# Kernel optimization log

Hardware: AMD Instinct MI355X
Metric: run time of the kernel (lower is better)

The kernel has to match this reference:

```python
import jax, jax.numpy as jnp
import numpy as np

NP_, NA_, NS_ = 4096, 4096, 1
E_ = 131072
DIN, DOUT, H = 256, 64, 4
SLOPE = 0.2  # leaky relu negative slope


def _leaky(x):
    return jnp.where(x >= 0, x, SLOPE * x)


def setup_inputs() -> dict:
    key = jax.random.key(0)
    ks = iter(jax.random.split(key, 64))
    inp = {}
    inp['feat_P'] = jax.random.normal(next(ks), (NP_, DIN), jnp.float32)
    inp['feat_A'] = jax.random.normal(next(ks), (NA_, DIN), jnp.float32)
    inp['feat_state'] = jax.random.normal(next(ks), (NS_, DIN), jnp.float32)
    for name in ['P', 'A', 'p2p', 'p2a', 'a2p', 'a2a', 'p2s', 'a2s', 'in']:
        inp['W_' + name] = jax.random.normal(next(ks), (DOUT * H, DIN), jnp.float32) / np.sqrt(DIN)
        inp['b_' + name] = jax.random.normal(next(ks), (DOUT * H,), jnp.float32) * 0.01
    for name in ['p2p', 'p2a', 'a2p', 'a2a', 'p2s', 'a2s']:
        inp['att_%s_src' % name] = jax.random.normal(next(ks), (1, H, DOUT), jnp.float32) * 0.1
        inp['att_%s_dst' % name] = jax.random.normal(next(ks), (1, H, DOUT), jnp.float32) * 0.1
    for name, ns, nd in [('p2p', NP_, NP_), ('p2a', NP_, NA_), ('a2p', NA_, NP_), ('a2a', NA_, NA_)]:
        inp['e_%s_src' % name] = jax.random.randint(next(ks), (E_,), 0, ns, jnp.int32)
        inp['e_%s_dst' % name] = jax.random.randint(next(ks), (E_,), 0, nd, jnp.int32)
    inp['e_p2s_src'] = jnp.arange(NP_, dtype=jnp.int32)
    inp['e_p2s_dst'] = jnp.zeros((NP_,), jnp.int32)
    inp['e_a2s_src'] = jnp.arange(NA_, dtype=jnp.int32)
    inp['e_a2s_dst'] = jnp.zeros((NA_,), jnp.int32)
    return inp


def _msg_agg(feat_src, W, b, att_s, att_d, Wh_dst, src, dst, n_dst):
    # per-edge lossy_u_mul_e with comm_loss == 0 (noise branch dead):
    # gather src features, per-edge linear, per-edge softmax over HEADS (torch Softmax(dim=1)).
    h = feat_src[src]                                    # [E, DIN]
    Wh = (h @ W.T + b).reshape(-1, H, DOUT)              # [E, H, D]
    a_s = jnp.sum(Wh * att_s, axis=-1, keepdims=True)    # [E, H, 1]
    a_d = jnp.sum(Wh_dst[dst] * att_d, axis=-1, keepdims=True)
    attn = jax.nn.softmax(_leaky(a_s + a_d), axis=1)     # softmax over heads, as in original
    return jax.ops.segment_sum(Wh * attn, dst, num_segments=n_dst)


def _edge_softmax_agg(Wh_src, att_s, Wh_state, att_d, src, dst, n_dst):
    # dgl edge_softmax: destination-grouped stable softmax over incoming edges.
    a_s = jnp.sum(Wh_src * att_s, axis=-1, keepdims=True)[src]    # [E, H, 1]
    a_d = jnp.sum(Wh_state * att_d, axis=-1, keepdims=True)[dst]  # [E, H, 1]
    e = _leaky(a_s + a_d)
    m = jax.ops.segment_max(e, dst, num_segments=n_dst)
    ex = jnp.exp(e - m[dst])
    den = jax.ops.segment_sum(ex, dst, num_segments=n_dst)
    a = ex / den[dst]
    return jax.ops.segment_sum(Wh_src[src] * a, dst, num_segments=n_dst)


def reference(feat_P, feat_A, feat_state,
              W_P, b_P, W_A, b_A, W_p2p, b_p2p, W_p2a, b_p2a, W_a2p, b_a2p,
              W_a2a, b_a2a, W_p2s, b_p2s, W_a2s, b_a2s, W_in, b_in,
              att_p2p_src, att_p2p_dst, att_p2a_src, att_p2a_dst,
              att_a2p_src, att_a2p_dst, att_a2a_src, att_a2a_dst,
              att_p2s_src, att_p2s_dst, att_a2s_src, att_a2s_dst,
              e_p2p_src, e_p2p_dst, e_p2a_src, e_p2a_dst,
              e_a2p_src, e_a2p_dst, e_a2a_src, e_a2a_dst,
              e_p2s_src, e_p2s_dst, e_a2s_src, e_a2s_dst):
    Whp = (feat_P @ W_P.T + b_P).reshape(NP_, H, DOUT)
    Wha = (feat_A @ W_A.T + b_A).reshape(NA_, H, DOUT)
    Whp2s = (feat_P @ W_p2s.T + b_p2s).reshape(NP_, H, DOUT)
    Wha2s = (feat_A @ W_a2s.T + b_a2s).reshape(NA_, H, DOUT)
    Whin = (feat_state @ W_in.T + b_in).reshape(NS_, H, DOUT)

    ft_p2p = _msg_agg(feat_P, W_p2p, b_p2p, att_p2p_src, att_p2p_dst, Whp, e_p2p_src, e_p2p_dst, NP_)
    ft_p2a = _msg_agg(feat_P, W_p2a, b_p2a, att_p2a_src, att_p2a_dst, Wha, e_p2a_src, e_p2a_dst, NA_)
    ft_a2p = _msg_agg(feat_A, W_a2p, b_a2p, att_a2p_src, att_a2p_dst, Whp, e_a2p_src, e_a2p_dst, NP_)
    ft_a2a = _msg_agg(feat_A, W_a2a, b_a2a, att_a2a_src, att_a2a_dst, Wha, e_a2a_src, e_a2a_dst, NA_)

    ft_p2s = _edge_softmax_agg(Whp2s, att_p2s_src, Whin, att_p2s_dst, e_p2s_src, e_p2s_dst, NS_)
    ft_a2s = _edge_softmax_agg(Wha2s, att_a2s_src, Whin, att_a2s_dst, e_a2s_src, e_a2s_dst, NS_)

    h_P = jax.nn.relu(Whp + ft_p2p + ft_a2p)
    h_A = jax.nn.relu(Wha + ft_p2a + ft_a2a)
    h_S = jax.nn.relu(Whin + ft_p2s + ft_a2s)
    return (h_P, h_A, h_S)
```

## Files before the change

### kernel.cpp

```cpp
#include <hip/hip_runtime.h>

#define NPA   4096
#define DHD   256
#define EDG   131072
#define OS    4104
#define TBL_SZ ((size_t)NPA * DHD)

#define B_AH    ((size_t)0)
#define B_WH    (B_AH + 2 * TBL_SZ * 2)
#define B_TBL   (B_WH + (size_t)8 * 65536 * 2)
#define B_SCORE (B_TBL + 8 * TBL_SZ * 2)
#define B_CNT   (B_SCORE + (size_t)10 * NPA * 4 * 4)
#define B_SCD   (B_CNT + (size_t)4 * NPA * 4)
#define B_DEN   (B_SCD + 8 * 4)
#define B_NUM   (B_DEN + 8 * 4)
#define B_ZEND  (B_NUM + 512 * 4)
#define B_OFFS  (B_ZEND)
#define B_CUR   (B_OFFS + (size_t)4 * OS * 4)
#define B_PKT   (B_CUR + (size_t)4 * NPA * 4)
#define B_WHIN  (B_PKT + (size_t)4 * EDG * 16)

typedef _Float16 half8 __attribute__((ext_vector_type(8)));
typedef _Float16 half4 __attribute__((ext_vector_type(4)));
typedef _Float16 half2v __attribute__((ext_vector_type(2)));
typedef float floatx4 __attribute__((ext_vector_type(4)));

struct CastArgs { const float* src[10]; };
struct GemmArgs {
    const float* b[8];
    const float* att0[8]; const float* att1[8];
    int sj0[8]; int sj1[8];
};
struct EdgeArgs { const int* src[4]; const int* dst[4]; };

__device__ __forceinline__ float lrelu(float x) { return x >= 0.0f ? x : 0.2f * x; }

__device__ __forceinline__ int pack2(float a, float b) {
    half2v h = {(_Float16)a, (_Float16)b};
    return __builtin_bit_cast(int, h);
}
__device__ __forceinline__ half2v bc2(int v) { return __builtin_bit_cast(half2v, v); }

__device__ __forceinline__ half2v asplat(const int4& p, int head) {
    int w = (head & 2) ? p.z : p.y;
    int b = (head & 1) ? ((w >> 16) & 0xffff) : (w & 0xffff);
    return bc2(b | (b << 16));
}

__global__ __launch_bounds__(256) void prep_kernel(CastArgs ca, EdgeArgs ea,
        const float* __restrict__ fs, const float* __restrict__ Win,
        const float* __restrict__ bin, const float* __restrict__ attP,
        const float* __restrict__ attA, _Float16* __restrict__ dst,
        int* __restrict__ cnt, float* __restrict__ whin, float* __restrict__ scd) {
    __shared__ int hist[NPA];
    int bid = blockIdx.x;
    int tid = threadIdx.x;
    if (bid < 32) {
        int r = bid >> 3;
        int chunk = bid & 7;
        const int* dp = ea.dst[r] + chunk * 16384;
#pragma unroll
        for (int i = 0; i < 16; ++i) hist[tid + i * 256] = 0;
        __syncthreads();
#pragma unroll
        for (int k = 0; k < 64; ++k)
            atomicAdd(&hist[dp[k * 256 + tid]], 1);
        __syncthreads();
        int* cr = cnt + r * NPA;
#pragma unroll
        for (int i = 0; i < 16; ++i) {
            int v = hist[tid + i * 256];
            if (v) atomicAdd(&cr[tid + i * 256], v);
        }
        return;
    }
    int wave = tid >> 6, lane = tid & 63;
    if (bid < 96) {
        int o = (bid - 32) * 4 + wave;
        float4 w = *(const float4*)&Win[(size_t)o * 256 + lane * 4];
        float4 f = *(const float4*)&fs[lane * 4];
        float v = w.x * f.x + w.y * f.y + w.z * f.z + w.w * f.w;
        for (int d = 32; d; d >>= 1) v += __shfl_xor(v, d);
        if (lane == 0) {
            v += bin[o];
            whin[o] = v;
            atomicAdd(&scd[o >> 6], v * attP[o]);
            atomicAdd(&scd[4 + (o >> 6)], v * attA[o]);
        }
        return;
    }
    size_t i4 = ((size_t)(bid - 96) * 256 + tid) * 4;
    const float* s; size_t off;
    if (i4 < TBL_SZ)            { s = ca.src[0]; off = i4; }
    else if (i4 < 2 * TBL_SZ)   { s = ca.src[1]; off = i4 - TBL_SZ; }
    else { size_t r = i4 - 2 * TBL_SZ; s = ca.src[2 + (r >> 16)]; off = r & 65535; }
    float4 v = *(const float4*)(s + off);
    half4 hh = {(_Float16)v.x, (_Float16)v.y, (_Float16)v.z, (_Float16)v.w};
    *(half4*)(dst + i4) = hh;
}

__global__ __launch_bounds__(256) void gemm_kernel(const _Float16* __restrict__ Ah,
        const _Float16* __restrict__ Whb, GemmArgs ga,
        _Float16* __restrict__ tblBase, float* __restrict__ score) {
    int j = blockIdx.x >> 6;
    int mt = blockIdx.x & 63;
    int w = threadIdx.x >> 6, lane = threadIdx.x & 63;
    int quad = lane >> 4, l16 = lane & 15;
    const _Float16* A = Ah + (size_t)(j >> 2) * TBL_SZ;
    const _Float16* W = Whb + (size_t)j * 65536;
    const float* bias = ga.b[j];
    _Float16* out = tblBase + (size_t)j * TBL_SZ;
    int mr0 = mt * 64;
    int nc0 = w * 64;
    const _Float16* ap[4];
    const _Float16* bp[4];
#pragma unroll
    for (int g = 0; g < 4; ++g) {
        ap[g] = A + (size_t)(mr0 + g * 16 + l16) * 256 + quad * 8;
        bp[g] = W + (size_t)(nc0 + g * 16 + l16) * 256 + quad * 8;
    }
    floatx4 acc[4][4];
#pragma unroll
    for (int rg = 0; rg < 4; ++rg)
#pragma unroll
        for (int cg = 0; cg < 4; ++cg) acc[rg][cg] = (floatx4){0, 0, 0, 0};
#pragma unroll
    for (int k0 = 0; k0 < 256; k0 += 32) {
        half8 av[4], bv[4];
#pragma unroll
        for (int g = 0; g < 4; ++g) av[g] = *(const half8*)(ap[g] + k0);
#pragma unroll
        for (int g = 0; g < 4; ++g) bv[g] = *(const half8*)(bp[g] + k0);
#pragma unroll
        for (int rg = 0; rg < 4; ++rg)
#pragma unroll
            for (int cg = 0; cg < 4; ++cg)
                acc[rg][cg] = __builtin_amdgcn_mfma_f32_16x16x32_f16(av[rg], bv[cg], acc[rg][cg], 0, 0, 0);
    }
    float bc[4];
#pragma unroll
    for (int cg = 0; cg < 4; ++cg) bc[cg] = bias[nc0 + cg * 16 + l16];
#pragma unroll
    for (int rg = 0; rg < 4; ++rg)
#pragma unroll
        for (int i = 0; i < 4; ++i) {
            int row = mr0 + rg * 16 + quad * 4 + i;
#pragma unroll
            for (int cg = 0; cg < 4; ++cg)
                out[(size_t)row * 256 + nc0 + cg * 16 + l16] = (_Float16)(acc[rg][cg][i] + bc[cg]);
        }
#pragma unroll
    for (int tt = 0; tt < 2; ++tt) {
        const float* att = tt ? ga.att1[j] : ga.att0[j];
        int sj = tt ? ga.sj1[j] : ga.sj0[j];
        if (!att) continue;
        float at[4];
#pragma unroll
        for (int cg = 0; cg < 4; ++cg) at[cg] = att[nc0 + cg * 16 + l16];
        float* sb = score + (size_t)sj * NPA * 4;
#pragma unroll
        for (int rg = 0; rg < 4; ++rg)
#pragma unroll
            for (int i = 0; i < 4; ++i) {
                float p = (acc[rg][0][i] + bc[0]) * at[0] + (acc[rg][1][i] + bc[1]) * at[1]
                        + (acc[rg][2][i] + bc[2]) * at[2] + (acc[rg][3][i] + bc[3]) * at[3];
                p += __shfl_xor(p, 1); p += __shfl_xor(p, 2);
                p += __shfl_xor(p, 4); p += __shfl_xor(p, 8);
                if (l16 == 0) {
                    int row = mr0 + rg * 16 + quad * 4 + i;
                    sb[(size_t)row * 4 + w] = p;
                }
            }
    }
}

__global__ __launch_bounds__(1024) void scan_kernel(const int* __restrict__ counts,
                                                    int* __restrict__ offs, int* __restrict__ cur) {
    int r = blockIdx.x;
    int t = threadIdx.x;
    int wave = t >> 6, lane = t & 63;
    int4 v = *(const int4*)&counts[(size_t)r * NPA + t * 4];
    int lsum = v.x + v.y + v.z + v.w;
    int s = lsum;
#pragma unroll
    for (int d = 1; d < 64; d <<= 1) {
        int u = __shfl_up(s, d);
        if (lane >= d) s += u;
    }
    __shared__ int wsum[16];
    if (lane == 63) wsum[wave] = s;
    __syncthreads();
    if (wave == 0 && lane < 16) {
        int wv = wsum[lane];
#pragma unroll
        for (int d = 1; d < 16; d <<= 1) {
            int u = __shfl_up(wv, d);
            if (lane >= d) wv += u;
        }
        wsum[lane] = wv;
    }
    __syncthreads();
    int base = (wave ? wsum[wave - 1] : 0) + s - lsum;
    int4 ov = {base, base + v.x, base + v.x + v.y, base + v.x + v.y + v.z};
    *(int4*)&offs[(size_t)r * OS + t * 4] = ov;
    *(int4*)&cur[(size_t)r * NPA + t * 4] = ov;
    if (t == 1023) offs[(size_t)r * OS + NPA] = base + lsum;
}

__global__ __launch_bounds__(256) void scatter_attn(EdgeArgs ea, const float* __restrict__ scoreBase,
        int* __restrict__ cur, int4* __restrict__ pkt) {
    int idx = (blockIdx.x * 256 + threadIdx.x) * 2;
    int r = idx >> 17;
    int e = idx & (EDG - 1);
    int2 s2 = *(const int2*)&ea.src[r][e];
    int2 d2 = *(const int2*)&ea.dst[r][e];
    const float* as = scoreBase + (size_t)r * NPA * 4;
    const float* ad = scoreBase + (size_t)(4 + r) * NPA * 4;
    float4 av0 = *(const float4*)&as[(size_t)s2.x * 4];
    float4 dv0 = *(const float4*)&ad[(size_t)d2.x * 4];
    float4 av1 = *(const float4*)&as[(size_t)s2.y * 4];
    float4 dv1 = *(const float4*)&ad[(size_t)d2.y * 4];
#pragma unroll
    for (int u = 0; u < 2; ++u) {
        float4 av = u ? av1 : av0;
        float4 dv = u ? dv1 : dv0;
        int s = u ? s2.y : s2.x;
        int d = u ? d2.y : d2.x;
        float x0 = lrelu(av.x + dv.x), x1 = lrelu(av.y + dv.y);
        float x2 = lrelu(av.z + dv.z), x3 = lrelu(av.w + dv.w);
        float m = fmaxf(fmaxf(x0, x1), fmaxf(x2, x3));
        float e0 = __expf(x0 - m), e1 = __expf(x1 - m), e2 = __expf(x2 - m), e3 = __expf(x3 - m);
        float inv = 1.0f / (e0 + e1 + e2 + e3);
        int pos = atomicAdd(&cur[r * NPA + d], 1);
        int4 pk = {s, pack2(e0 * inv, e1 * inv), pack2(e2 * inv, e3 * inv), 0};
        pkt[(size_t)r * EDG + pos] = pk;
    }
}

__global__ __launch_bounds__(256) void agg_kernel(const int* __restrict__ offs,
        const int4* __restrict__ pkt, const _Float16* __restrict__ tblBase,
        float* __restrict__ outBase) {
    int side = blockIdx.y;
    int wave = threadIdx.x >> 6, lane = threadIdx.x & 63;
    int dn = blockIdx.x * 4 + wave;
    int h = lane >> 5, l32 = lane & 31;
    int head = l32 >> 3;
    half2v accA[4] = {{0,0},{0,0},{0,0},{0,0}};
    half2v accB[4] = {{0,0},{0,0},{0,0},{0,0}};
    const int srcIdx[4] = {1, 2, 5, 6};
    const int4 z = {0, 0, 0, 0};
#pragma unroll
    for (int q = 0; q < 2; ++q) {
        int r = side + q * 2;
        const int* of = offs + (size_t)r * OS;
        const int4* pkb = pkt + (size_t)r * EDG;
        const _Float16* wh = tblBase + (size_t)srcIdx[r] * TBL_SZ;
        int beg = of[dn], end = of[dn + 1];
        int i = beg;
        int4 p0 = (i + h     < end) ? pkb[i + h]     : z;
        int4 p1 = (i + 2 + h < end) ? pkb[i + 2 + h] : z;
        int4 p2 = (i + 4 + h < end) ? pkb[i + 4 + h] : z;
        int4 p3 = (i + 6 + h < end) ? pkb[i + 6 + h] : z;
        while (i < end) {
            int ni = i + 8;
            half8 w0 = *(const half8*)(wh + (size_t)p0.x * 256 + l32 * 8);
            half8 w1 = *(const half8*)(wh + (size_t)p1.x * 256 + l32 * 8);
            half8 w2 = *(const half8*)(wh + (size_t)p2.x * 256 + l32 * 8);
            half8 w3 = *(const half8*)(wh + (size_t)p3.x * 256 + l32 * 8);
            int4 n0 = (ni + h     < end) ? pkb[ni + h]     : z;
            int4 n1 = (ni + 2 + h < end) ? pkb[ni + 2 + h] : z;
            int4 n2 = (ni + 4 + h < end) ? pkb[ni + 4 + h] : z;
            int4 n3 = (ni + 6 + h < end) ? pkb[ni + 6 + h] : z;
            half2v a0 = asplat(p0, head), a1 = asplat(p1, head);
            half2v a2 = asplat(p2, head), a3 = asplat(p3, head);
            int4 i0 = __builtin_bit_cast(int4, w0);
            int4 i1 = __builtin_bit_cast(int4, w1);
            int4 i2 = __builtin_bit_cast(int4, w2);
            int4 i3 = __builtin_bit_cast(int4, w3);
            accA[0] += bc2(i0.x) * a0; accA[1] += bc2(i0.y) * a0;
            accA[2] += bc2(i0.z) * a0; accA[3] += bc2(i0.w) * a0;
            accB[0] += bc2(i1.x) * a1; accB[1] += bc2(i1.y) * a1;
            accB[2] += bc2(i1.z) * a1; accB[3] += bc2(i1.w) * a1;
            accA[0] += bc2(i2.x) * a2; accA[1] += bc2(i2.y) * a2;
            accA[2] += bc2(i2.z) * a2; accA[3] += bc2(i2.w) * a2;
            accB[0] += bc2(i3.x) * a3; accB[1] += bc2(i3.y) * a3;
            accB[2] += bc2(i3.z) * a3; accB[3] += bc2(i3.w) * a3;
            p0 = n0; p1 = n1; p2 = n2; p3 = n3;
            i = ni;
        }
    }
    float f[8];
#pragma unroll
    for (int k = 0; k < 4; ++k) {
        half2v s = accA[k] + accB[k];
        f[2 * k] = (float)s[0];
        f[2 * k + 1] = (float)s[1];
    }
#pragma unroll
    for (int k = 0; k < 8; ++k) f[k] += __shfl_xor(f[k], 32);
    if (h == 0) {
        const _Float16* skip = tblBase + (size_t)(side * 4) * TBL_SZ + (size_t)dn * 256 + l32 * 8;
        half8 sv = *(const half8*)skip;
        float* op = outBase + ((size_t)side * NPA + dn) * 256 + l32 * 8;
        float4 o0 = {fmaxf(f[0] + (float)sv[0], 0.f), fmaxf(f[1] + (float)sv[1], 0.f),
                     fmaxf(f[2] + (float)sv[2], 0.f), fmaxf(f[3] + (float)sv[3], 0.f)};
        float4 o1 = {fmaxf(f[4] + (float)sv[4], 0.f), fmaxf(f[5] + (float)sv[5], 0.f),
                     fmaxf(f[6] + (float)sv[6], 0.f), fmaxf(f[7] + (float)sv[7], 0.f)};
        *(float4*)op = o0;
        *(float4*)(op + 4) = o1;
    }
}

__global__ __launch_bounds__(256) void state_kernel(const _Float16* __restrict__ tblBase,
        const float* __restrict__ scoreBase, const float* __restrict__ scd,
        float* __restrict__ den, float* __restrict__ num) {
    int r = blockIdx.y;
    int blk = blockIdx.x;
    int t = threadIdx.x;
    int h = t >> 6;
    const _Float16* wh = tblBase + (size_t)(r == 0 ? 3 : 7) * TBL_SZ;
    const float* as = scoreBase + (size_t)(8 + r) * NPA * 4;
    float dh = scd[r * 4 + h];
    float dsum = 0.0f, acc = 0.0f;
    for (int i = blk; i < NPA; i += 128) {
        float x = lrelu(as[(size_t)i * 4 + h] + dh);
        float w = __expf(x);
        dsum += w;
        acc += w * (float)wh[(size_t)i * 256 + t];
    }
    atomicAdd(&num[r * 256 + t], acc);
    if ((t & 63) == 0) atomicAdd(&den[r * 4 + h], dsum);
}

__global__ __launch_bounds__(256) void state_final(const float* __restrict__ whin,
        const float* __restrict__ den, const float* __restrict__ num, float* __restrict__ out) {
    int t = threadIdx.x;
    int h = t >> 6;
    float v = whin[t] + num[t] / den[h] + num[256 + t] / den[4 + h];
    out[t] = v > 0.0f ? v : 0.0f;
}

extern "C" void kernel_launch(void* const* d_in, const int* in_sizes, int n_in,
                              void* d_out, int out_size, void* d_ws, size_t ws_size,
                              hipStream_t stream) {
    auto F = [&](int i) { return (const float*)d_in[i]; };
    char* ws = (char*)d_ws;
    _Float16* Ah  = (_Float16*)(ws + B_AH);
    _Float16* Whb = (_Float16*)(ws + B_WH);
    _Float16* tbl = (_Float16*)(ws + B_TBL);
    float* score  = (float*)(ws + B_SCORE);
    int* cnt      = (int*)(ws + B_CNT);
    float* scd    = (float*)(ws + B_SCD);
    float* den    = (float*)(ws + B_DEN);
    float* num    = (float*)(ws + B_NUM);
    int* offs     = (int*)(ws + B_OFFS);
    int* cur      = (int*)(ws + B_CUR);
    int4* pkt     = (int4*)(ws + B_PKT);
    float* whin   = (float*)(ws + B_WHIN);

    (void)hipMemsetAsync(ws + B_CNT, 0, B_ZEND - B_CNT, stream);

    CastArgs ca = {{F(0), F(1), F(3), F(7), F(9), F(15), F(5), F(11), F(13), F(17)}};
    EdgeArgs ea = {{(const int*)d_in[33], (const int*)d_in[35], (const int*)d_in[37], (const int*)d_in[39]},
                   {(const int*)d_in[34], (const int*)d_in[36], (const int*)d_in[38], (const int*)d_in[40]}};

    prep_kernel<<<2656, 256, 0, stream>>>(ca, ea, F(2), F(19), F(20), F(30), F(32),
                                          Ah, cnt, whin, scd);

    GemmArgs ga;
    const int bIdx[8] = {4, 8, 10, 16, 6, 12, 14, 18};
    for (int j = 0; j < 8; ++j) ga.b[j] = F(bIdx[j]);
    const int a0Idx[8]  = {22, 21, 23, 29, 24, 25, 27, 31};
    const int sj0Arr[8] = { 4,  0,  1,  8,  5,  2,  3,  9};
    for (int j = 0; j < 8; ++j) {
        ga.att0[j] = F(a0Idx[j]); ga.sj0[j] = sj0Arr[j];
        ga.att1[j] = nullptr;     ga.sj1[j] = -1;
    }
    ga.att1[0] = F(26); ga.sj1[0] = 6;
    ga.att1[4] = F(28); ga.sj1[4] = 7;

    gemm_kernel<<<512, 256, 0, stream>>>(Ah, Whb, ga, tbl, score);
    scan_kernel<<<4, 1024, 0, stream>>>(cnt, offs, cur);
    scatter_attn<<<1024, 256, 0, stream>>>(ea, score, cur, pkt);
    agg_kernel<<<dim3(1024, 2), 256, 0, stream>>>(offs, pkt, tbl, (float*)d_out);
    state_kernel<<<dim3(128, 2), 256, 0, stream>>>(tbl, score, scd, den, num);
    state_final<<<1, 256, 0, stream>>>(whin, den, num, (float*)d_out + 2 * TBL_SZ);
}
```

Measured before the change: 269.6 us.

## Fuse scan into GEMM, state into scatter/agg, drop memset and global atomics

Cuts the launch count from seven (memset plus six kernels) to four by merging kernels. The edge-count scan now runs inside the GEMM launch, the state reduction inside the scatter launch, and the state finalize inside the aggregation launch. Per-block histograms and partial state sums are written to private slots instead of being combined with global atomics, which removes the memset. The GEMM M-tile is halved to 32 rows, giving 1024 blocks for more parallelism. The trade-offs are extra partial-sum reads in the finalize step and the state-vector dot product shrinking to a single block.

```diff
diff --git a/kernel.cpp b/kernel.cpp
--- a/kernel.cpp
+++ b/kernel.cpp
@@ -4,21 +4,21 @@
 #define DHD   256
 #define EDG   131072
 #define OS    4104
+#define PST   64
 #define TBL_SZ ((size_t)NPA * DHD)
 
 #define B_AH    ((size_t)0)
 #define B_WH    (B_AH + 2 * TBL_SZ * 2)
 #define B_TBL   (B_WH + (size_t)8 * 65536 * 2)
 #define B_SCORE (B_TBL + 8 * TBL_SZ * 2)
-#define B_CNT   (B_SCORE + (size_t)10 * NPA * 4 * 4)
-#define B_SCD   (B_CNT + (size_t)4 * NPA * 4)
-#define B_DEN   (B_SCD + 8 * 4)
-#define B_NUM   (B_DEN + 8 * 4)
-#define B_ZEND  (B_NUM + 512 * 4)
-#define B_OFFS  (B_ZEND)
+#define B_CNTP  (B_SCORE + (size_t)10 * NPA * 4 * 4)
+#define B_OFFS  (B_CNTP + (size_t)32 * NPA * 4)
 #define B_CUR   (B_OFFS + (size_t)4 * OS * 4)
 #define B_PKT   (B_CUR + (size_t)4 * NPA * 4)
 #define B_WHIN  (B_PKT + (size_t)4 * EDG * 16)
+#define B_SCD   (B_WHIN + 256 * 4)
+#define B_NUMP  (B_SCD + 8 * 4)
+#define B_DENP  (B_NUMP + (size_t)2 * PST * 256 * 4)
 
 typedef _Float16 half8 __attribute__((ext_vector_type(8)));
 typedef _Float16 half4 __attribute__((ext_vector_type(4)));
@@ -51,7 +51,7 @@
         const float* __restrict__ fs, const float* __restrict__ Win,
         const float* __restrict__ bin, const float* __restrict__ attP,
         const float* __restrict__ attA, _Float16* __restrict__ dst,
-        int* __restrict__ cnt, float* __restrict__ whin, float* __restrict__ scd) {
+        int* __restrict__ cntp, float* __restrict__ whin, float* __restrict__ scd) {
     __shared__ int hist[NPA];
     int bid = blockIdx.x;
     int tid = threadIdx.x;
@@ -66,30 +66,30 @@
         for (int k = 0; k < 64; ++k)
             atomicAdd(&hist[dp[k * 256 + tid]], 1);
         __syncthreads();
-        int* cr = cnt + r * NPA;
-#pragma unroll
-        for (int i = 0; i < 16; ++i) {
-            int v = hist[tid + i * 256];
-            if (v) atomicAdd(&cr[tid + i * 256], v);
-        }
+        int* cr = cntp + (size_t)bid * NPA;
+#pragma unroll
+        for (int i = 0; i < 16; ++i)
+            cr[tid + i * 256] = hist[tid + i * 256];
         return;
     }
     int wave = tid >> 6, lane = tid & 63;
-    if (bid < 96) {
-        int o = (bid - 32) * 4 + wave;
-        float4 w = *(const float4*)&Win[(size_t)o * 256 + lane * 4];
-        float4 f = *(const float4*)&fs[lane * 4];
-        float v = w.x * f.x + w.y * f.y + w.z * f.z + w.w * f.w;
-        for (int d = 32; d; d >>= 1) v += __shfl_xor(v, d);
-        if (lane == 0) {
+    if (bid == 32) {
+        float sp = 0.f, sa = 0.f;
+        for (int k = 0; k < 64; ++k) {
+            int o = wave * 64 + k;
+            float4 w = *(const float4*)&Win[(size_t)o * 256 + lane * 4];
+            float4 f = *(const float4*)&fs[lane * 4];
+            float v = w.x * f.x + w.y * f.y + w.z * f.z + w.w * f.w;
+            for (int d = 32; d; d >>= 1) v += __shfl_xor(v, d);
             v += bin[o];
-            whin[o] = v;
-            atomicAdd(&scd[o >> 6], v * attP[o]);
-            atomicAdd(&scd[4 + (o >> 6)], v * attA[o]);
-        }
+            if (lane == 0) whin[o] = v;
+            sp += v * attP[o];
+            sa += v * attA[o];
+        }
+        if (lane == 0) { scd[wave] = sp; scd[4 + wave] = sa; }
         return;
     }
-    size_t i4 = ((size_t)(bid - 96) * 256 + tid) * 4;
+    size_t i4 = ((size_t)(bid - 33) * 256 + tid) * 4;
     const float* s; size_t off;
     if (i4 < TBL_SZ)            { s = ca.src[0]; off = i4; }
     else if (i4 < 2 * TBL_SZ)   { s = ca.src[1]; off = i4 - TBL_SZ; }
@@ -99,40 +99,90 @@
     *(half4*)(dst + i4) = hh;
 }
 
-__global__ __launch_bounds__(256) void gemm_kernel(const _Float16* __restrict__ Ah,
-        const _Float16* __restrict__ Whb, GemmArgs ga,
-        _Float16* __restrict__ tblBase, float* __restrict__ score) {
-    int j = blockIdx.x >> 6;
-    int mt = blockIdx.x & 63;
-    int w = threadIdx.x >> 6, lane = threadIdx.x & 63;
+__global__ __launch_bounds__(256) void gemm_scan(const _Float16* __restrict__ Ah,
+        const _Float16* __restrict__ Whb, GemmArgs ga, const int* __restrict__ cntp,
+        _Float16* __restrict__ tblBase, float* __restrict__ score,
+        int* __restrict__ offs, int* __restrict__ cur) {
+    int bid = blockIdx.x;
+    int t = threadIdx.x;
+    if (bid < 4) {
+        int r = bid;
+        int4 s[4];
+#pragma unroll
+        for (int q = 0; q < 4; ++q) {
+            int4 acc = {0, 0, 0, 0};
+#pragma unroll
+            for (int b = 0; b < 8; ++b) {
+                const int4* cp = (const int4*)(cntp + (size_t)(r * 8 + b) * NPA);
+                int4 u = cp[t * 4 + q];
+                acc.x += u.x; acc.y += u.y; acc.z += u.z; acc.w += u.w;
+            }
+            s[q] = acc;
+        }
+        int lsum = 0;
+#pragma unroll
+        for (int q = 0; q < 4; ++q) lsum += s[q].x + s[q].y + s[q].z + s[q].w;
+        int wave = t >> 6, lane = t & 63;
+        int sc = lsum;
+#pragma unroll
+        for (int d = 1; d < 64; d <<= 1) {
+            int u = __shfl_up(sc, d);
+            if (lane >= d) sc += u;
+        }
+        __shared__ int ws4[4];
+        if (lane == 63) ws4[wave] = sc;
+        __syncthreads();
+        int wb = 0;
+        for (int w = 0; w < 4; ++w) if (w < wave) wb += ws4[w];
+        int run = wb + sc - lsum;
+        int* of = offs + (size_t)r * OS;
+        int* cu = cur + (size_t)r * NPA;
+#pragma unroll
+        for (int q = 0; q < 4; ++q) {
+            int4 o;
+            o.x = run; run += s[q].x;
+            o.y = run; run += s[q].y;
+            o.z = run; run += s[q].z;
+            o.w = run; run += s[q].w;
+            ((int4*)of)[t * 4 + q] = o;
+            ((int4*)cu)[t * 4 + q] = o;
+        }
+        if (t == 255) of[NPA] = run;
+        return;
+    }
+    int g = bid - 4;
+    int j = g >> 7;
+    int mt = g & 127;
+    int w = t >> 6, lane = t & 63;
     int quad = lane >> 4, l16 = lane & 15;
     const _Float16* A = Ah + (size_t)(j >> 2) * TBL_SZ;
     const _Float16* W = Whb + (size_t)j * 65536;
     const float* bias = ga.b[j];
     _Float16* out = tblBase + (size_t)j * TBL_SZ;
-    int mr0 = mt * 64;
+    int mr0 = mt * 32;
     int nc0 = w * 64;
-    const _Float16* ap[4];
+    const _Float16* ap[2];
     const _Float16* bp[4];
 #pragma unroll
-    for (int g = 0; g < 4; ++g) {
-        ap[g] = A + (size_t)(mr0 + g * 16 + l16) * 256 + quad * 8;
-        bp[g] = W + (size_t)(nc0 + g * 16 + l16) * 256 + quad * 8;
-    }
-    floatx4 acc[4][4];
-#pragma unroll
-    for (int rg = 0; rg < 4; ++rg)
+    for (int g2 = 0; g2 < 2; ++g2)
+        ap[g2] = A + (size_t)(mr0 + g2 * 16 + l16) * 256 + quad * 8;
+#pragma unroll
+    for (int g2 = 0; g2 < 4; ++g2)
+        bp[g2] = W + (size_t)(nc0 + g2 * 16 + l16) * 256 + quad * 8;
+    floatx4 acc[2][4];
+#pragma unroll
+    for (int rg = 0; rg < 2; ++rg)
 #pragma unroll
         for (int cg = 0; cg < 4; ++cg) acc[rg][cg] = (floatx4){0, 0, 0, 0};
 #pragma unroll
     for (int k0 = 0; k0 < 256; k0 += 32) {
-        half8 av[4], bv[4];
-#pragma unroll
-        for (int g = 0; g < 4; ++g) av[g] = *(const half8*)(ap[g] + k0);
-#pragma unroll
-        for (int g = 0; g < 4; ++g) bv[g] = *(const half8*)(bp[g] + k0);
-#pragma unroll
-        for (int rg = 0; rg < 4; ++rg)
+        half8 av[2], bv[4];
+#pragma unroll
+        for (int g2 = 0; g2 < 2; ++g2) av[g2] = *(const half8*)(ap[g2] + k0);
+#pragma unroll
+        for (int g2 = 0; g2 < 4; ++g2) bv[g2] = *(const half8*)(bp[g2] + k0);
+#pragma unroll
+        for (int rg = 0; rg < 2; ++rg)
 #pragma unroll
             for (int cg = 0; cg < 4; ++cg)
                 acc[rg][cg] = __builtin_amdgcn_mfma_f32_16x16x32_f16(av[rg], bv[cg], acc[rg][cg], 0, 0, 0);
@@ -141,7 +191,7 @@
 #pragma unroll
     for (int cg = 0; cg < 4; ++cg) bc[cg] = bias[nc0 + cg * 16 + l16];
 #pragma unroll
-    for (int rg = 0; rg < 4; ++rg)
+    for (int rg = 0; rg < 2; ++rg)
 #pragma unroll
         for (int i = 0; i < 4; ++i) {
             int row = mr0 + rg * 16 + quad * 4 + i;
@@ -159,7 +209,7 @@
         for (int cg = 0; cg < 4; ++cg) at[cg] = att[nc0 + cg * 16 + l16];
         float* sb = score + (size_t)sj * NPA * 4;
 #pragma unroll
-        for (int rg = 0; rg < 4; ++rg)
+        for (int rg = 0; rg < 2; ++rg)
 #pragma unroll
             for (int i = 0; i < 4; ++i) {
                 float p = (acc[rg][0][i] + bc[0]) * at[0] + (acc[rg][1][i] + bc[1]) * at[1]
@@ -174,48 +224,38 @@
     }
 }
 
-__global__ __launch_bounds__(1024) void scan_kernel(const int* __restrict__ counts,
-                                                    int* __restrict__ offs, int* __restrict__ cur) {
-    int r = blockIdx.x;
+__global__ __launch_bounds__(256) void scatter_state(EdgeArgs ea,
+        const float* __restrict__ score, int* __restrict__ cur, int4* __restrict__ pkt,
+        const _Float16* __restrict__ tblBase, const float* __restrict__ scd,
+        float* __restrict__ numP, float* __restrict__ denP) {
+    int bid = blockIdx.x;
     int t = threadIdx.x;
-    int wave = t >> 6, lane = t & 63;
-    int4 v = *(const int4*)&counts[(size_t)r * NPA + t * 4];
-    int lsum = v.x + v.y + v.z + v.w;
-    int s = lsum;
-#pragma unroll
-    for (int d = 1; d < 64; d <<= 1) {
-        int u = __shfl_up(s, d);
-        if (lane >= d) s += u;
-    }
-    __shared__ int wsum[16];
-    if (lane == 63) wsum[wave] = s;
-    __syncthreads();
-    if (wave == 0 && lane < 16) {
-        int wv = wsum[lane];
-#pragma unroll
-        for (int d = 1; d < 16; d <<= 1) {
-            int u = __shfl_up(wv, d);
-            if (lane >= d) wv += u;
-        }
-        wsum[lane] = wv;
-    }
-    __syncthreads();
-    int base = (wave ? wsum[wave - 1] : 0) + s - lsum;
-    int4 ov = {base, base + v.x, base + v.x + v.y, base + v.x + v.y + v.z};
-    *(int4*)&offs[(size_t)r * OS + t * 4] = ov;
-    *(int4*)&cur[(size_t)r * NPA + t * 4] = ov;
-    if (t == 1023) offs[(size_t)r * OS + NPA] = base + lsum;
-}
-
-__global__ __launch_bounds__(256) void scatter_attn(EdgeArgs ea, const float* __restrict__ scoreBase,
-        int* __restrict__ cur, int4* __restrict__ pkt) {
-    int idx = (blockIdx.x * 256 + threadIdx.x) * 2;
+    if (bid >= 1024) {
+        int sb = bid - 1024;
+        int r = sb >> 6;
+        int blk = sb & 63;
+        int h = t >> 6;
+        const _Float16* wh = tblBase + (size_t)(r == 0 ? 3 : 7) * TBL_SZ;
+        const float* as = score + (size_t)(8 + r) * NPA * 4;
+        float dh = scd[r * 4 + h];
+        float dsum = 0.0f, acc = 0.0f;
+        for (int i = blk; i < NPA; i += PST) {
+            float x = lrelu(as[(size_t)i * 4 + h] + dh);
+            float w = __expf(x);
+            dsum += w;
+            acc += w * (float)wh[(size_t)i * 256 + t];
+        }
+        numP[(size_t)(r * PST + blk) * 256 + t] = acc;
+        if ((t & 63) == 0) denP[(size_t)(r * PST + blk) * 4 + h] = dsum;
+        return;
+    }
+    int idx = (bid * 256 + t) * 2;
     int r = idx >> 17;
     int e = idx & (EDG - 1);
     int2 s2 = *(const int2*)&ea.src[r][e];
     int2 d2 = *(const int2*)&ea.dst[r][e];
-    const float* as = scoreBase + (size_t)r * NPA * 4;
-    const float* ad = scoreBase + (size_t)(4 + r) * NPA * 4;
+    const float* as = score + (size_t)r * NPA * 4;
+    const float* ad = score + (size_t)(4 + r) * NPA * 4;
     float4 av0 = *(const float4*)&as[(size_t)s2.x * 4];
     float4 dv0 = *(const float4*)&ad[(size_t)d2.x * 4];
     float4 av1 = *(const float4*)&as[(size_t)s2.y * 4];
@@ -237,12 +277,30 @@
     }
 }
 
-__global__ __launch_bounds__(256) void agg_kernel(const int* __restrict__ offs,
+__global__ __launch_bounds__(256) void agg_final(const int* __restrict__ offs,
         const int4* __restrict__ pkt, const _Float16* __restrict__ tblBase,
-        float* __restrict__ outBase) {
-    int side = blockIdx.y;
-    int wave = threadIdx.x >> 6, lane = threadIdx.x & 63;
-    int dn = blockIdx.x * 4 + wave;
+        const float* __restrict__ whin, const float* __restrict__ numP,
+        const float* __restrict__ denP, float* __restrict__ outBase) {
+    int bid = blockIdx.x;
+    int tid = threadIdx.x;
+    if (bid == 2048) {
+        int t = tid;
+        int h = t >> 6;
+        float n0 = 0.f, n1 = 0.f, d0 = 0.f, d1 = 0.f;
+        for (int b = 0; b < PST; ++b) {
+            n0 += numP[(size_t)b * 256 + t];
+            n1 += numP[(size_t)(PST + b) * 256 + t];
+            d0 += denP[(size_t)b * 4 + h];
+            d1 += denP[(size_t)(PST + b) * 4 + h];
+        }
+        float v = whin[t] + n0 / d0 + n1 / d1;
+        outBase[2 * TBL_SZ + t] = fmaxf(v, 0.f);
+        return;
+    }
+    int side = bid >> 10;
+    int bx = bid & 1023;
+    int wave = tid >> 6, lane = tid & 63;
+    int dn = bx * 4 + wave;
     int h = lane >> 5, l32 = lane & 31;
     int head = l32 >> 3;
     half2v accA[4] = {{0,0},{0,0},{0,0},{0,0}};
@@ -311,35 +369,6 @@
     }
 }
 
-__global__ __launch_bounds__(256) void state_kernel(const _Float16* __restrict__ tblBase,
-        const float* __restrict__ scoreBase, const float* __restrict__ scd,
-        float* __restrict__ den, float* __restrict__ num) {
-    int r = blockIdx.y;
-    int blk = blockIdx.x;
-    int t = threadIdx.x;
-    int h = t >> 6;
-    const _Float16* wh = tblBase + (size_t)(r == 0 ? 3 : 7) * TBL_SZ;
-    const float* as = scoreBase + (size_t)(8 + r) * NPA * 4;
-    float dh = scd[r * 4 + h];
-    float dsum = 0.0f, acc = 0.0f;
-    for (int i = blk; i < NPA; i += 128) {
-        float x = lrelu(as[(size_t)i * 4 + h] + dh);
-        float w = __expf(x);
-        dsum += w;
-        acc += w * (float)wh[(size_t)i * 256 + t];
-    }
-    atomicAdd(&num[r * 256 + t], acc);
-    if ((t & 63) == 0) atomicAdd(&den[r * 4 + h], dsum);
-}
-
-__global__ __launch_bounds__(256) void state_final(const float* __restrict__ whin,
-        const float* __restrict__ den, const float* __restrict__ num, float* __restrict__ out) {
-    int t = threadIdx.x;
-    int h = t >> 6;
-    float v = whin[t] + num[t] / den[h] + num[256 + t] / den[4 + h];
-    out[t] = v > 0.0f ? v : 0.0f;
-}
-
 extern "C" void kernel_launch(void* const* d_in, const int* in_sizes, int n_in,
                               void* d_out, int out_size, void* d_ws, size_t ws_size,
                               hipStream_t stream) {
@@ -349,23 +378,21 @@
     _Float16* Whb = (_Float16*)(ws + B_WH);
     _Float16* tbl = (_Float16*)(ws + B_TBL);
     float* score  = (float*)(ws + B_SCORE);
-    int* cnt      = (int*)(ws + B_CNT);
-    float* scd    = (float*)(ws + B_SCD);
-    float* den    = (float*)(ws + B_DEN);
-    float* num    = (float*)(ws + B_NUM);
+    int* cntp     = (int*)(ws + B_CNTP);
     int* offs     = (int*)(ws + B_OFFS);
     int* cur      = (int*)(ws + B_CUR);
     int4* pkt     = (int4*)(ws + B_PKT);
     float* whin   = (float*)(ws + B_WHIN);
-
-    (void)hipMemsetAsync(ws + B_CNT, 0, B_ZEND - B_CNT, stream);
+    float* scd    = (float*)(ws + B_SCD);
+    float* numP   = (float*)(ws + B_NUMP);
+    float* denP   = (float*)(ws + B_DENP);
 
     CastArgs ca = {{F(0), F(1), F(3), F(7), F(9), F(15), F(5), F(11), F(13), F(17)}};
     EdgeArgs ea = {{(const int*)d_in[33], (const int*)d_in[35], (const int*)d_in[37], (const int*)d_in[39]},
                    {(const int*)d_in[34], (const int*)d_in[36], (const int*)d_in[38], (const int*)d_in[40]}};
 
-    prep_kernel<<<2656, 256, 0, stream>>>(ca, ea, F(2), F(19), F(20), F(30), F(32),
-                                          Ah, cnt, whin, scd);
+    prep_kernel<<<2593, 256, 0, stream>>>(ca, ea, F(2), F(19), F(20), F(30), F(32),
+                                          Ah, cntp, whin, scd);
 
     GemmArgs ga;
     const int bIdx[8] = {4, 8, 10, 16, 6, 12, 14, 18};
@@ -379,10 +406,7 @@
     ga.att1[0] = F(26); ga.sj1[0] = 6;
     ga.att1[4] = F(28); ga.sj1[4] = 7;
 
-    gemm_kernel<<<512, 256, 0, stream>>>(Ah, Whb, ga, tbl, score);
-    scan_kernel<<<4, 1024, 0, stream>>>(cnt, offs, cur);
-    scatter_attn<<<1024, 256, 0, stream>>>(ea, score, cur, pkt);
-    agg_kernel<<<dim3(1024, 2), 256, 0, stream>>>(offs, pkt, tbl, (float*)d_out);
-    state_kernel<<<dim3(128, 2), 256, 0, stream>>>(tbl, score, scd, den, num);
-    state_final<<<1, 256, 0, stream>>>(whin, den, num, (float*)d_out + 2 * TBL_SZ);
-}
+    gemm_scan<<<4 + 1024, 256, 0, stream>>>(Ah, Whb, ga, cntp, tbl, score, offs, cur);
+    scatter_state<<<1024 + 2 * PST, 256, 0, stream>>>(ea, score, cur, pkt, tbl, scd, numP, denP);
+    agg_final<<<2049, 256, 0, stream>>>(offs, pkt, tbl, whin, numP, denP, (float*)d_out);
+}
```

New measurement: 281.2 us. 4.3% more time.
